# Performance work log

Measured on AMD Instinct MI355X. Metric: run time of the kernel, lower is better.

Reference implementation:

```python
import jax, jax.numpy as jnp
import numpy as np

DIM = 512
NUM_HEADS = 8
HEAD_DIM = DIM // NUM_HEADS
SCALE = HEAD_DIM ** -0.5


def setup_inputs() -> dict:
    key = jax.random.key(0)
    k_x, k_wqkv, k_bqkv, k_wp, k_bp = jax.random.split(key, 5)
    x = jax.random.normal(k_x, (2, 4096, DIM), dtype=jnp.float32)
    s = DIM ** -0.5
    W_qkv = jax.random.normal(k_wqkv, (DIM, 3 * DIM), dtype=jnp.float32) * s
    b_qkv = jax.random.normal(k_bqkv, (3 * DIM,), dtype=jnp.float32) * 0.02
    W_proj = jax.random.normal(k_wp, (DIM, DIM), dtype=jnp.float32) * s
    b_proj = jax.random.normal(k_bp, (DIM,), dtype=jnp.float32) * 0.02
    return {"x": x, "W_qkv": W_qkv, "b_qkv": b_qkv, "W_proj": W_proj, "b_proj": b_proj}


def reference(x, W_qkv, b_qkv, W_proj, b_proj):
    B, S, D = x.shape
    H, Hd = NUM_HEADS, HEAD_DIM
    qkv = x @ W_qkv + b_qkv                      # [B, S, 3D]
    qkv = qkv.reshape(B, S, 3, H, Hd)
    q, k, v = jnp.moveaxis(qkv, 2, 0)            # each [B, S, H, Hd]
    # scores: [B, H, S, S] (explicit, matching the original non-fused impl)
    attn = jnp.einsum('bshd,bthd->bhst', q, k) * SCALE
    attn = jax.nn.softmax(attn, axis=-1)
    out = jnp.einsum('bhst,bthd->bshd', attn, v) # [B, S, H, Hd]
    out = out.reshape(B, S, D)
    return out @ W_proj + b_proj
```

## Files before the change

### kernel.cpp

```cpp
#include <hip/hip_runtime.h>
#include <hip/hip_bf16.h>
#include <stdint.h>

typedef __attribute__((ext_vector_type(8))) short bf16x8;
typedef __attribute__((ext_vector_type(4))) float f32x4;
typedef __attribute__((ext_vector_type(4))) int i32x4;

__device__ __forceinline__ short f2bf(float f) {
  uint32_t u = __builtin_bit_cast(uint32_t, f);
  u = u + 0x7FFFu + ((u >> 16) & 1u);
  return (short)(u >> 16);
}


__global__ __launch_bounds__(256) void convert_x_kernel(const float* __restrict__ x,
                                                        short* __restrict__ xb) {
  int i = (blockIdx.x * 256 + threadIdx.x) * 8;
  float4 v0 = *(const float4*)(x + i);
  float4 v1 = *(const float4*)(x + i + 4);
  uint32_t p0 = (uint16_t)f2bf(v0.x) | ((uint32_t)(uint16_t)f2bf(v0.y) << 16);
  uint32_t p1 = (uint16_t)f2bf(v0.z) | ((uint32_t)(uint16_t)f2bf(v0.w) << 16);
  uint32_t p2 = (uint16_t)f2bf(v1.x) | ((uint32_t)(uint16_t)f2bf(v1.y) << 16);
  uint32_t p3 = (uint16_t)f2bf(v1.z) | ((uint32_t)(uint16_t)f2bf(v1.w) << 16);
  i32x4 o = {(int)p0, (int)p1, (int)p2, (int)p3};
  *(i32x4*)(xb + i) = o;
}

__global__ __launch_bounds__(256) void transpose_w_kernel(const float* __restrict__ W,
                                                          short* __restrict__ Wt, int N) {
  int idx = blockIdx.x * 256 + threadIdx.x;
  int n = idx >> 9, k = idx & 511;
  Wt[idx] = f2bf(W[(size_t)k * N + n]);
}


__global__ __launch_bounds__(256) void gemm_qkv_kernel(const short* __restrict__ A,
                                                       const short* __restrict__ Bt,
                                                       const float* __restrict__ bias,
                                                       short* __restrict__ Qb,
                                                       short* __restrict__ Kb,
                                                       short* __restrict__ Vt) {
  __shared__ short Al[128 * 32];
  __shared__ short Bl[128 * 32];
  const int tid = threadIdx.x;
  const int bm = (blockIdx.x & 63) << 7;
  const int bn = (blockIdx.x >> 6) << 7;
  const int lane = tid & 63;
  const int wv = tid >> 6;
  const int wm = (wv >> 1) * 64, wn = (wv & 1) * 64;
  const int lr = lane & 15, lg = lane >> 4;

  f32x4 acc[4][4];
#pragma unroll
  for (int i = 0; i < 4; i++)
#pragma unroll
    for (int j = 0; j < 4; j++) acc[i][j] = (f32x4){0.f, 0.f, 0.f, 0.f};

  for (int k0 = 0; k0 < 512; k0 += 32) {
    __syncthreads();
#pragma unroll
    for (int i = 0; i < 2; ++i) {
      int c = tid + i * 256;
      int row = c >> 2, coff = (c & 3) * 8;
      *(i32x4*)(&Al[row * 32 + coff]) = *(const i32x4*)(A + (size_t)(bm + row) * 512 + k0 + coff);
      *(i32x4*)(&Bl[row * 32 + coff]) = *(const i32x4*)(Bt + (size_t)(bn + row) * 512 + k0 + coff);
    }
    __syncthreads();
    bf16x8 a[4], b[4];
#pragma unroll
    for (int mi = 0; mi < 4; mi++) a[mi] = *(const bf16x8*)(&Al[(wm + mi * 16 + lr) * 32 + lg * 8]);
#pragma unroll
    for (int ni = 0; ni < 4; ni++) b[ni] = *(const bf16x8*)(&Bl[(wn + ni * 16 + lr) * 32 + lg * 8]);
#pragma unroll
    for (int mi = 0; mi < 4; mi++)
#pragma unroll
      for (int ni = 0; ni < 4; ni++)
        acc[mi][ni] = __builtin_amdgcn_mfma_f32_16x16x32_bf16(a[mi], b[ni], acc[mi][ni], 0, 0, 0);
  }

#pragma unroll
  for (int ni = 0; ni < 4; ni++) {
    int n = bn + wn + ni * 16 + lr;
    float bv = bias[n];
    int three = n >> 9, hn = n & 511;
    int h = hn >> 6, d = hn & 63;
#pragma unroll
    for (int mi = 0; mi < 4; mi++) {
#pragma unroll
      for (int r = 0; r < 4; r++) {
        int m = bm + wm + mi * 16 + lg * 4 + r;
        int bb = m >> 12, s = m & 4095;
        float v = acc[mi][ni][r] + bv;
        int bh = bb * 8 + h;
        if (three == 0) {
          Qb[((size_t)bh * 4096 + s) * 64 + d] = f2bf(v * 0.125f);
        } else if (three == 1) {
          Kb[((size_t)bh * 4096 + s) * 64 + d] = f2bf(v);
        } else {
          Vt[((size_t)bh * 64 + d) * 4096 + s] = f2bf(v);
        }
      }
    }
  }
}


__global__ __launch_bounds__(256, 4) void attn_kernel(const short* __restrict__ Qb,
                                                      const short* __restrict__ Kb,
                                                      const short* __restrict__ Vt,
                                                      short* __restrict__ Ob) {
  __shared__ short Kl[2][64 * 64];
  __shared__ short Vl[2][64 * 64];
  __shared__ short Pl[4][16 * 64];

  const int tid = threadIdx.x;
  const int lane = tid & 63;
  const int wv = tid >> 6;
  const int lr = lane & 15, lg = lane >> 4;
  const int b = blockIdx.x;
  const int qt = (b >> 3) & 63;
  const int bh = (b & 7) | ((b >> 9) << 3);

  const int qrow = qt * 64 + wv * 16 + lr;
  const size_t qbase = ((size_t)bh * 4096 + qrow) * 64;
  const bf16x8 qf0 = *(const bf16x8*)(Qb + qbase + lg * 8);
  const bf16x8 qf1 = *(const bf16x8*)(Qb + qbase + 32 + lg * 8);

  const short one_bf = (short)0x3F80;
  const bf16x8 onesf = {one_bf, one_bf, one_bf, one_bf, one_bf, one_bf, one_bf, one_bf};

  float m_run = -1e30f;
  f32x4 ol = (f32x4){0.f, 0.f, 0.f, 0.f};
  f32x4 o[4];
#pragma unroll
  for (int nt = 0; nt < 4; nt++) o[nt] = (f32x4){0.f, 0.f, 0.f, 0.f};

  const size_t kgbase = (size_t)bh * 4096 * 64;
  const size_t vgbase = (size_t)bh * 64 * 4096;
  short* Pw = &Pl[wv][0];

  const int srow = lane >> 3;
  const int schunk = ((lane & 7) ^ srow) * 8;
  const int li0 = wv * 2;

  auto stage = [&](int buf, int kb_) {
#pragma unroll
    for (int i = 0; i < 2; i++) {
      const int li = li0 + i;
      const int row = li * 8 + srow;
      __builtin_amdgcn_global_load_lds(
          (const __attribute__((address_space(1))) void*)(Kb + kgbase + (size_t)(kb_ + row) * 64 + schunk),
          (__attribute__((address_space(3))) void*)(&Kl[buf][li * 512]), 16, 0, 0);
      __builtin_amdgcn_global_load_lds(
          (const __attribute__((address_space(1))) void*)(Vt + vgbase + (size_t)row * 4096 + kb_ + schunk),
          (__attribute__((address_space(3))) void*)(&Vl[buf][li * 512]), 16, 0, 0);
    }
  };

  stage(0, 0);
  __syncthreads();
  int cur = 0;

  for (int kb = 0; kb < 4096; kb += 64) {
    if (kb + 64 < 4096) stage(cur ^ 1, kb + 64);

    const short* Kc = &Kl[cur][0];
    const short* Vc = &Vl[cur][0];
    const int sw = (lr & 7) << 4;

    f32x4 st[4];
#pragma unroll
    for (int kt = 0; kt < 4; kt++) {
      const int key = kt * 16 + lr;
      const char* krow = (const char*)Kc + key * 128;
      bf16x8 b0 = *(const bf16x8*)(krow + ((lg * 16) ^ sw));
      bf16x8 b1 = *(const bf16x8*)(krow + ((64 + lg * 16) ^ sw));
      f32x4 s = (f32x4){0.f, 0.f, 0.f, 0.f};
      s = __builtin_amdgcn_mfma_f32_16x16x32_bf16(qf0, b0, s, 0, 0, 0);
      s = __builtin_amdgcn_mfma_f32_16x16x32_bf16(qf1, b1, s, 0, 0, 0);
      st[kt] = s;
    }

    float cm = fmaxf(fmaxf(st[0][0], st[0][1]), fmaxf(st[0][2], st[0][3]));
#pragma unroll
    for (int kt = 1; kt < 4; kt++)
      cm = fmaxf(cm, fmaxf(fmaxf(st[kt][0], st[kt][1]), fmaxf(st[kt][2], st[kt][3])));
#pragma unroll
    for (int off = 1; off < 64; off <<= 1) cm = fmaxf(cm, __shfl_xor(cm, off, 64));

    if (cm > m_run) {
      float fac = exp2f((m_run - cm) * 1.44269504f);
      m_run = cm;
#pragma unroll
      for (int nt = 0; nt < 4; nt++)
#pragma unroll
        for (int r = 0; r < 4; r++) o[nt][r] *= fac;
#pragma unroll
      for (int r = 0; r < 4; r++) ol[r] *= fac;
    }
    const float mb = m_run * 1.44269504f;

#pragma unroll
    for (int kt = 0; kt < 4; kt++)
#pragma unroll
      for (int r = 0; r < 4; r++) {
        float p = exp2f(__builtin_fmaf(st[kt][r], 1.44269504f, -mb));
        const int R = lg * 4 + r;
        const int pos = (kt * 2 + (lr >> 3)) ^ (R & 7);
        Pw[R * 64 + pos * 8 + (lr & 7)] = f2bf(p);
      }

    bf16x8 pf0 = *(const bf16x8*)(Pw + lr * 64 + ((lg ^ (lr & 7)) * 8));
    bf16x8 pf1 = *(const bf16x8*)(Pw + lr * 64 + (((4 + lg) ^ (lr & 7)) * 8));

#pragma unroll
    for (int nt = 0; nt < 4; nt++) {
      const int d = nt * 16 + lr;
      const char* vrow = (const char*)Vc + d * 128;
      bf16x8 v0 = *(const bf16x8*)(vrow + ((lg * 16) ^ sw));
      bf16x8 v1 = *(const bf16x8*)(vrow + ((64 + lg * 16) ^ sw));
      o[nt] = __builtin_amdgcn_mfma_f32_16x16x32_bf16(pf0, v0, o[nt], 0, 0, 0);
      o[nt] = __builtin_amdgcn_mfma_f32_16x16x32_bf16(pf1, v1, o[nt], 0, 0, 0);
    }
    ol = __builtin_amdgcn_mfma_f32_16x16x32_bf16(pf0, onesf, ol, 0, 0, 0);
    ol = __builtin_amdgcn_mfma_f32_16x16x32_bf16(pf1, onesf, ol, 0, 0, 0);

    __syncthreads();
    cur ^= 1;
  }

  const int bb = bh >> 3, h = bh & 7;
#pragma unroll
  for (int r = 0; r < 4; r++) {
    float inv = 1.f / ol[r];
    int s = qt * 64 + wv * 16 + lg * 4 + r;
    size_t rowb = ((size_t)bb * 4096 + s) * 512 + h * 64;
#pragma unroll
    for (int nt = 0; nt < 4; nt++) Ob[rowb + nt * 16 + lr] = f2bf(o[nt][r] * inv);
  }
}


__global__ __launch_bounds__(256) void gemm_proj_kernel(const short* __restrict__ A,
                                                        const short* __restrict__ Bt,
                                                        const float* __restrict__ bias,
                                                        float* __restrict__ out) {
  __shared__ short Al[128 * 32];
  __shared__ short Bl[128 * 32];
  const int tid = threadIdx.x;
  const int bm = (blockIdx.x & 63) << 7;
  const int bn = (blockIdx.x >> 6) << 7;
  const int lane = tid & 63;
  const int wv = tid >> 6;
  const int wm = (wv >> 1) * 64, wn = (wv & 1) * 64;
  const int lr = lane & 15, lg = lane >> 4;

  f32x4 acc[4][4];
#pragma unroll
  for (int i = 0; i < 4; i++)
#pragma unroll
    for (int j = 0; j < 4; j++) acc[i][j] = (f32x4){0.f, 0.f, 0.f, 0.f};

  for (int k0 = 0; k0 < 512; k0 += 32) {
    __syncthreads();
#pragma unroll
    for (int i = 0; i < 2; ++i) {
      int c = tid + i * 256;
      int row = c >> 2, coff = (c & 3) * 8;
      *(i32x4*)(&Al[row * 32 + coff]) = *(const i32x4*)(A + (size_t)(bm + row) * 512 + k0 + coff);
      *(i32x4*)(&Bl[row * 32 + coff]) = *(const i32x4*)(Bt + (size_t)(bn + row) * 512 + k0 + coff);
    }
    __syncthreads();
    bf16x8 a[4], b[4];
#pragma unroll
    for (int mi = 0; mi < 4; mi++) a[mi] = *(const bf16x8*)(&Al[(wm + mi * 16 + lr) * 32 + lg * 8]);
#pragma unroll
    for (int ni = 0; ni < 4; ni++) b[ni] = *(const bf16x8*)(&Bl[(wn + ni * 16 + lr) * 32 + lg * 8]);
#pragma unroll
    for (int mi = 0; mi < 4; mi++)
#pragma unroll
      for (int ni = 0; ni < 4; ni++)
        acc[mi][ni] = __builtin_amdgcn_mfma_f32_16x16x32_bf16(a[mi], b[ni], acc[mi][ni], 0, 0, 0);
  }

#pragma unroll
  for (int ni = 0; ni < 4; ni++) {
    int n = bn + wn + ni * 16 + lr;
    float bv = bias[n];
#pragma unroll
    for (int mi = 0; mi < 4; mi++) {
#pragma unroll
      for (int r = 0; r < 4; r++) {
        int m = bm + wm + mi * 16 + lg * 4 + r;
        out[(size_t)m * 512 + n] = acc[mi][ni][r] + bv;
      }
    }
  }
}


extern "C" void kernel_launch(void* const* d_in, const int* in_sizes, int n_in,
                              void* d_out, int out_size, void* d_ws, size_t ws_size,
                              hipStream_t stream) {
  const float* x = (const float*)d_in[0];
  const float* Wqkv = (const float*)d_in[1];
  const float* bqkv = (const float*)d_in[2];
  const float* Wproj = (const float*)d_in[3];
  const float* bproj = (const float*)d_in[4];
  float* out = (float*)d_out;

  char* ws = (char*)d_ws;
  short* xb  = (short*)(ws);
  short* Wqt = (short*)(ws + 8388608);
  short* Wpt = (short*)(ws + 9961472);
  short* Qb  = (short*)(ws + 10485760);
  short* Kb  = (short*)(ws + 18874368);
  short* Vt  = (short*)(ws + 27262976);
  short* Ob  = (short*)(ws + 35651584);

  convert_x_kernel<<<2048, 256, 0, stream>>>(x, xb);
  transpose_w_kernel<<<3072, 256, 0, stream>>>(Wqkv, Wqt, 1536);
  transpose_w_kernel<<<1024, 256, 0, stream>>>(Wproj, Wpt, 512);
  gemm_qkv_kernel<<<768, 256, 0, stream>>>(xb, Wqt, bqkv, Qb, Kb, Vt);
  attn_kernel<<<1024, 256, 0, stream>>>(Qb, Kb, Vt, Ob);
  gemm_proj_kernel<<<256, 256, 0, stream>>>(Ob, Wpt, bproj, out);
}
```

Measured before the change: 281.3 us.

## Rework attention with 32x32 MFMA, register-resident P, lazy rescale; tile weight transpose

The attention kernel now uses 32x32x16 MFMAs with 128-query tiles per block (32 per wave), computing S transposed so P stays in registers via packed bf16 converts and lane shuffles instead of an LDS round trip. The row sum is accumulated with plain adds instead of an MFMA against ones, and rescaling is skipped unless the running max grows by more than a threshold. The weight transpose becomes an LDS-tiled coalesced kernel, and both GEMMs load their tiles with direct global-to-LDS loads. Halving the grid and the occupancy hint lowers parallelism, and the lazy max threshold relies on fp32 headroom for the unnormalised exponentials.

Measured after the change: 256.2 us. 1.1x faster.

```diff
diff --git a/kernel.cpp b/kernel.cpp
--- a/kernel.cpp
+++ b/kernel.cpp
@@ -4,6 +4,7 @@
 
 typedef __attribute__((ext_vector_type(8))) short bf16x8;
 typedef __attribute__((ext_vector_type(4))) float f32x4;
+typedef __attribute__((ext_vector_type(16))) float f32x16;
 typedef __attribute__((ext_vector_type(4))) int i32x4;
 
 __device__ __forceinline__ short f2bf(float f) {
@@ -27,10 +28,25 @@
 }
 
 __global__ __launch_bounds__(256) void transpose_w_kernel(const float* __restrict__ W,
-                                                          short* __restrict__ Wt, int N) {
-  int idx = blockIdx.x * 256 + threadIdx.x;
-  int n = idx >> 9, k = idx & 511;
-  Wt[idx] = f2bf(W[(size_t)k * N + n]);
+                                                          short* __restrict__ Wt, int N,
+                                                          int nTilesN) {
+  __shared__ short Ts[64 * 66];
+  const int t = threadIdx.x;
+  const int n0 = (blockIdx.x % nTilesN) * 64;
+  const int k0 = (blockIdx.x / nTilesN) * 64;
+#pragma unroll
+  for (int j = 0; j < 16; j++) {
+    int e = j * 256 + t;
+    int k = e >> 6, n = e & 63;
+    Ts[k * 66 + n] = f2bf(W[(size_t)(k0 + k) * N + n0 + n]);
+  }
+  __syncthreads();
+#pragma unroll
+  for (int j = 0; j < 16; j++) {
+    int e = j * 256 + t;
+    int n = e >> 6, k = e & 63;
+    Wt[(size_t)(n0 + n) * 512 + k0 + k] = Ts[k * 66 + n];
+  }
 }
 
 
@@ -62,8 +78,12 @@
     for (int i = 0; i < 2; ++i) {
       int c = tid + i * 256;
       int row = c >> 2, coff = (c & 3) * 8;
-      *(i32x4*)(&Al[row * 32 + coff]) = *(const i32x4*)(A + (size_t)(bm + row) * 512 + k0 + coff);
-      *(i32x4*)(&Bl[row * 32 + coff]) = *(const i32x4*)(Bt + (size_t)(bn + row) * 512 + k0 + coff);
+      __builtin_amdgcn_global_load_lds(
+          (const __attribute__((address_space(1))) void*)(A + (size_t)(bm + row) * 512 + k0 + coff),
+          (__attribute__((address_space(3))) void*)(&Al[c * 8]), 16, 0, 0);
+      __builtin_amdgcn_global_load_lds(
+          (const __attribute__((address_space(1))) void*)(Bt + (size_t)(bn + row) * 512 + k0 + coff),
+          (__attribute__((address_space(3))) void*)(&Bl[c * 8]), 16, 0, 0);
     }
     __syncthreads();
     bf16x8 a[4], b[4];
@@ -105,39 +125,34 @@
 }
 
 
-__global__ __launch_bounds__(256, 4) void attn_kernel(const short* __restrict__ Qb,
+__global__ __launch_bounds__(256, 2) void attn_kernel(const short* __restrict__ Qb,
                                                       const short* __restrict__ Kb,
                                                       const short* __restrict__ Vt,
                                                       short* __restrict__ Ob) {
   __shared__ short Kl[2][64 * 64];
   __shared__ short Vl[2][64 * 64];
-  __shared__ short Pl[4][16 * 64];
 
   const int tid = threadIdx.x;
   const int lane = tid & 63;
   const int wv = tid >> 6;
-  const int lr = lane & 15, lg = lane >> 4;
+  const int q5 = lane & 31, h = lane >> 5;
   const int b = blockIdx.x;
-  const int qt = (b >> 3) & 63;
-  const int bh = (b & 7) | ((b >> 9) << 3);
-
-  const int qrow = qt * 64 + wv * 16 + lr;
-  const size_t qbase = ((size_t)bh * 4096 + qrow) * 64;
-  const bf16x8 qf0 = *(const bf16x8*)(Qb + qbase + lg * 8);
-  const bf16x8 qf1 = *(const bf16x8*)(Qb + qbase + 32 + lg * 8);
-
-  const short one_bf = (short)0x3F80;
-  const bf16x8 onesf = {one_bf, one_bf, one_bf, one_bf, one_bf, one_bf, one_bf, one_bf};
-
-  float m_run = -1e30f;
-  f32x4 ol = (f32x4){0.f, 0.f, 0.f, 0.f};
-  f32x4 o[4];
-#pragma unroll
-  for (int nt = 0; nt < 4; nt++) o[nt] = (f32x4){0.f, 0.f, 0.f, 0.f};
+  const int qt = (b >> 3) & 31;
+  const int bh = (b & 7) | ((b >> 8) << 3);
+
+  const int qrow = qt * 128 + wv * 32 + q5;
+  const short* Qrow = Qb + ((size_t)bh * 4096 + qrow) * 64;
+  bf16x8 qf[4];
+#pragma unroll
+  for (int c = 0; c < 4; c++) qf[c] = *(const bf16x8*)(Qrow + c * 16 + h * 8);
+
+  float m_run = -1e30f, l_run = 0.f;
+  f32x16 oA, oB;
+#pragma unroll
+  for (int r = 0; r < 16; r++) { oA[r] = 0.f; oB[r] = 0.f; }
 
   const size_t kgbase = (size_t)bh * 4096 * 64;
   const size_t vgbase = (size_t)bh * 64 * 4096;
-  short* Pw = &Pl[wv][0];
 
   const int srow = lane >> 3;
   const int schunk = ((lane & 7) ^ srow) * 8;
@@ -161,82 +176,107 @@
   __syncthreads();
   int cur = 0;
 
+  const int vsw = (q5 & 7) << 4;
+
   for (int kb = 0; kb < 4096; kb += 64) {
     if (kb + 64 < 4096) stage(cur ^ 1, kb + 64);
-
     const short* Kc = &Kl[cur][0];
     const short* Vc = &Vl[cur][0];
-    const int sw = (lr & 7) << 4;
-
-    f32x4 st[4];
-#pragma unroll
-    for (int kt = 0; kt < 4; kt++) {
-      const int key = kt * 16 + lr;
-      const char* krow = (const char*)Kc + key * 128;
-      bf16x8 b0 = *(const bf16x8*)(krow + ((lg * 16) ^ sw));
-      bf16x8 b1 = *(const bf16x8*)(krow + ((64 + lg * 16) ^ sw));
-      f32x4 s = (f32x4){0.f, 0.f, 0.f, 0.f};
-      s = __builtin_amdgcn_mfma_f32_16x16x32_bf16(qf0, b0, s, 0, 0, 0);
-      s = __builtin_amdgcn_mfma_f32_16x16x32_bf16(qf1, b1, s, 0, 0, 0);
-      st[kt] = s;
-    }
-
-    float cm = fmaxf(fmaxf(st[0][0], st[0][1]), fmaxf(st[0][2], st[0][3]));
-#pragma unroll
-    for (int kt = 1; kt < 4; kt++)
-      cm = fmaxf(cm, fmaxf(fmaxf(st[kt][0], st[kt][1]), fmaxf(st[kt][2], st[kt][3])));
-#pragma unroll
-    for (int off = 1; off < 64; off <<= 1) cm = fmaxf(cm, __shfl_xor(cm, off, 64));
-
-    if (cm > m_run) {
-      float fac = exp2f((m_run - cm) * 1.44269504f);
-      m_run = cm;
-#pragma unroll
-      for (int nt = 0; nt < 4; nt++)
-#pragma unroll
-        for (int r = 0; r < 4; r++) o[nt][r] *= fac;
-#pragma unroll
-      for (int r = 0; r < 4; r++) ol[r] *= fac;
-    }
-    const float mb = m_run * 1.44269504f;
-
-#pragma unroll
-    for (int kt = 0; kt < 4; kt++)
-#pragma unroll
-      for (int r = 0; r < 4; r++) {
-        float p = exp2f(__builtin_fmaf(st[kt][r], 1.44269504f, -mb));
-        const int R = lg * 4 + r;
-        const int pos = (kt * 2 + (lr >> 3)) ^ (R & 7);
-        Pw[R * 64 + pos * 8 + (lr & 7)] = f2bf(p);
-      }
-
-    bf16x8 pf0 = *(const bf16x8*)(Pw + lr * 64 + ((lg ^ (lr & 7)) * 8));
-    bf16x8 pf1 = *(const bf16x8*)(Pw + lr * 64 + (((4 + lg) ^ (lr & 7)) * 8));
-
-#pragma unroll
-    for (int nt = 0; nt < 4; nt++) {
-      const int d = nt * 16 + lr;
-      const char* vrow = (const char*)Vc + d * 128;
-      bf16x8 v0 = *(const bf16x8*)(vrow + ((lg * 16) ^ sw));
-      bf16x8 v1 = *(const bf16x8*)(vrow + ((64 + lg * 16) ^ sw));
-      o[nt] = __builtin_amdgcn_mfma_f32_16x16x32_bf16(pf0, v0, o[nt], 0, 0, 0);
-      o[nt] = __builtin_amdgcn_mfma_f32_16x16x32_bf16(pf1, v1, o[nt], 0, 0, 0);
-    }
-    ol = __builtin_amdgcn_mfma_f32_16x16x32_bf16(pf0, onesf, ol, 0, 0, 0);
-    ol = __builtin_amdgcn_mfma_f32_16x16x32_bf16(pf1, onesf, ol, 0, 0, 0);
+
+#pragma unroll
+    for (int ks = 0; ks < 2; ks++) {
+      f32x16 sc;
+#pragma unroll
+      for (int r = 0; r < 16; r++) sc[r] = 0.f;
+      {
+        const int krow = ks * 32 + q5;
+        const char* kbase = (const char*)Kc + krow * 128;
+        const int ksw = (krow & 7) << 4;
+#pragma unroll
+        for (int c = 0; c < 4; c++) {
+          bf16x8 kf = *(const bf16x8*)(kbase + ((((c << 1) + h) << 4) ^ ksw));
+          sc = __builtin_amdgcn_mfma_f32_32x32x16_bf16(kf, qf[c], sc, 0, 0, 0);
+        }
+      }
+
+      float pm = sc[0];
+#pragma unroll
+      for (int r = 1; r < 16; r++) pm = fmaxf(pm, sc[r]);
+      pm = fmaxf(pm, __shfl_xor(pm, 32, 64));
+
+      if (!__all(pm <= m_run + 8.0f)) {
+        float nm = fmaxf(m_run, pm);
+        float fac = exp2f((m_run - nm) * 1.44269504f);
+        m_run = nm;
+        l_run *= fac;
+#pragma unroll
+        for (int r = 0; r < 16; r++) {
+          const int qm = (r & 3) + 8 * (r >> 2);
+          float fr = __shfl(fac, qm + (h << 2), 64);
+          oA[r] *= fr;
+          oB[r] *= fr;
+        }
+      }
+
+      const float mb = m_run * 1.44269504f;
+      float p[16];
+      float ls = 0.f;
+#pragma unroll
+      for (int r = 0; r < 16; r++) {
+        p[r] = exp2f(__builtin_fmaf(sc[r], 1.44269504f, -mb));
+        ls += p[r];
+      }
+      ls += __shfl_xor(ls, 32, 64);
+      l_run += ls;
+
+      uint32_t w0, w1, w2, w3, w4, w5, w6, w7;
+      asm("v_cvt_pk_bf16_f32 %0, %1, %2" : "=v"(w0) : "v"(p[0]), "v"(p[1]));
+      asm("v_cvt_pk_bf16_f32 %0, %1, %2" : "=v"(w1) : "v"(p[2]), "v"(p[3]));
+      asm("v_cvt_pk_bf16_f32 %0, %1, %2" : "=v"(w2) : "v"(p[4]), "v"(p[5]));
+      asm("v_cvt_pk_bf16_f32 %0, %1, %2" : "=v"(w3) : "v"(p[6]), "v"(p[7]));
+      asm("v_cvt_pk_bf16_f32 %0, %1, %2" : "=v"(w4) : "v"(p[8]), "v"(p[9]));
+      asm("v_cvt_pk_bf16_f32 %0, %1, %2" : "=v"(w5) : "v"(p[10]), "v"(p[11]));
+      asm("v_cvt_pk_bf16_f32 %0, %1, %2" : "=v"(w6) : "v"(p[12]), "v"(p[13]));
+      asm("v_cvt_pk_bf16_f32 %0, %1, %2" : "=v"(w7) : "v"(p[14]), "v"(p[15]));
+      uint32_t e0 = (uint32_t)__shfl_xor((int)(h ? w0 : w2), 32, 64);
+      uint32_t e1 = (uint32_t)__shfl_xor((int)(h ? w1 : w3), 32, 64);
+      uint32_t e2 = (uint32_t)__shfl_xor((int)(h ? w4 : w6), 32, 64);
+      uint32_t e3 = (uint32_t)__shfl_xor((int)(h ? w5 : w7), 32, 64);
+      i32x4 fa0 = {(int)(h ? e0 : w0), (int)(h ? e1 : w1), (int)(h ? w2 : e0), (int)(h ? w3 : e1)};
+      i32x4 fa1 = {(int)(h ? e2 : w4), (int)(h ? e3 : w5), (int)(h ? w6 : e2), (int)(h ? w7 : e3)};
+      bf16x8 pa0 = __builtin_bit_cast(bf16x8, fa0);
+      bf16x8 pa1 = __builtin_bit_cast(bf16x8, fa1);
+
+      {
+        const char* vb0 = (const char*)Vc + q5 * 128;
+        const char* vb1 = vb0 + 32 * 128;
+        const int c0 = ((ks * 4 + h) << 4) ^ vsw;
+        const int c1 = ((ks * 4 + 2 + h) << 4) ^ vsw;
+        bf16x8 va00 = *(const bf16x8*)(vb0 + c0);
+        bf16x8 va01 = *(const bf16x8*)(vb0 + c1);
+        bf16x8 va10 = *(const bf16x8*)(vb1 + c0);
+        bf16x8 va11 = *(const bf16x8*)(vb1 + c1);
+        oA = __builtin_amdgcn_mfma_f32_32x32x16_bf16(pa0, va00, oA, 0, 0, 0);
+        oA = __builtin_amdgcn_mfma_f32_32x32x16_bf16(pa1, va01, oA, 0, 0, 0);
+        oB = __builtin_amdgcn_mfma_f32_32x32x16_bf16(pa0, va10, oB, 0, 0, 0);
+        oB = __builtin_amdgcn_mfma_f32_32x32x16_bf16(pa1, va11, oB, 0, 0, 0);
+      }
+    }
 
     __syncthreads();
     cur ^= 1;
   }
 
-  const int bb = bh >> 3, h = bh & 7;
-#pragma unroll
-  for (int r = 0; r < 4; r++) {
-    float inv = 1.f / ol[r];
-    int s = qt * 64 + wv * 16 + lg * 4 + r;
-    size_t rowb = ((size_t)bb * 4096 + s) * 512 + h * 64;
-#pragma unroll
-    for (int nt = 0; nt < 4; nt++) Ob[rowb + nt * 16 + lr] = f2bf(o[nt][r] * inv);
+  const int bb = bh >> 3, hh = bh & 7;
+  float linv = 1.0f / l_run;
+#pragma unroll
+  for (int r = 0; r < 16; r++) {
+    const int qm = (r & 3) + 8 * (r >> 2);
+    float li = __shfl(linv, qm + (h << 2), 64);
+    int orow = qt * 128 + wv * 32 + qm + 4 * h;
+    size_t rowb = ((size_t)bb * 4096 + orow) * 512 + hh * 64;
+    Ob[rowb + q5] = f2bf(oA[r] * li);
+    Ob[rowb + 32 + q5] = f2bf(oB[r] * li);
   }
 }
 
@@ -267,8 +307,12 @@
     for (int i = 0; i < 2; ++i) {
       int c = tid + i * 256;
       int row = c >> 2, coff = (c & 3) * 8;
-      *(i32x4*)(&Al[row * 32 + coff]) = *(const i32x4*)(A + (size_t)(bm + row) * 512 + k0 + coff);
-      *(i32x4*)(&Bl[row * 32 + coff]) = *(const i32x4*)(Bt + (size_t)(bn + row) * 512 + k0 + coff);
+      __builtin_amdgcn_global_load_lds(
+          (const __attribute__((address_space(1))) void*)(A + (size_t)(bm + row) * 512 + k0 + coff),
+          (__attribute__((address_space(3))) void*)(&Al[c * 8]), 16, 0, 0);
+      __builtin_amdgcn_global_load_lds(
+          (const __attribute__((address_space(1))) void*)(Bt + (size_t)(bn + row) * 512 + k0 + coff),
+          (__attribute__((address_space(3))) void*)(&Bl[c * 8]), 16, 0, 0);
     }
     __syncthreads();
     bf16x8 a[4], b[4];
@@ -319,9 +363,9 @@
   short* Ob  = (short*)(ws + 35651584);
 
   convert_x_kernel<<<2048, 256, 0, stream>>>(x, xb);
-  transpose_w_kernel<<<3072, 256, 0, stream>>>(Wqkv, Wqt, 1536);
-  transpose_w_kernel<<<1024, 256, 0, stream>>>(Wproj, Wpt, 512);
+  transpose_w_kernel<<<192, 256, 0, stream>>>(Wqkv, Wqt, 1536, 24);
+  transpose_w_kernel<<<64, 256, 0, stream>>>(Wproj, Wpt, 512, 8);
   gemm_qkv_kernel<<<768, 256, 0, stream>>>(xb, Wqt, bqkv, Qb, Kb, Vt);
-  attn_kernel<<<1024, 256, 0, stream>>>(Qb, Kb, Vt, Ob);
+  attn_kernel<<<512, 256, 0, stream>>>(Qb, Kb, Vt, Ob);
   gemm_proj_kernel<<<256, 256, 0, stream>>>(Ob, Wpt, bproj, out);
 }
```
